# Performance work log

Measured on AMD Instinct MI355X. Metric: run time of the kernel, lower is better.

Reference implementation:

```python
import jax, jax.numpy as jnp
import numpy as np

N_USERS = 100000
N_MOVIES = 20000
N_EDGES = 600000
FEAT = 64
HID = 128
OUT = 64
N_TUPLES = 100000


def _sage(x_src, x_dst, src_idx, dst_idx, n_dst, Wl, bl, Wr):
    # PyG SAGEConv (mean aggr): lin_l(mean of gathered src feats) + lin_r(x_dst)
    msg = x_src[src_idx]                                        # [E, d_src]
    summ = jax.ops.segment_sum(msg, dst_idx, num_segments=n_dst)
    cnt = jax.ops.segment_sum(jnp.ones((src_idx.shape[0],), x_src.dtype),
                              dst_idx, num_segments=n_dst)
    mean = summ / jnp.maximum(cnt, 1.0)[:, None]
    return mean @ Wl.T + bl + x_dst @ Wr.T


def setup_inputs() -> dict:
    key = jax.random.key(0)
    ks = jax.random.split(key, 20)
    s = 0.05
    return {
        "movie_x": jax.random.normal(ks[0], (N_MOVIES, FEAT), jnp.float32),
        "user_idx": jax.random.randint(ks[1], (N_EDGES,), 0, N_USERS),
        "movie_idx": jax.random.randint(ks[2], (N_EDGES,), 0, N_MOVIES),
        "tuples_coo": jax.random.randint(ks[3], (2, N_TUPLES), 0, N_MOVIES),
        "user_emb": jax.random.normal(ks[4], (1, HID), jnp.float32) * s,
        "W1l": jax.random.normal(ks[5], (HID, FEAT), jnp.float32) * s,
        "b1": jnp.zeros((HID,), jnp.float32),
        "W1r": jax.random.normal(ks[6], (HID, HID), jnp.float32) * s,
        "W2l": jax.random.normal(ks[7], (HID, HID), jnp.float32) * s,
        "b2": jnp.zeros((HID,), jnp.float32),
        "W2r": jax.random.normal(ks[8], (HID, FEAT), jnp.float32) * s,
        "W3l": jax.random.normal(ks[9], (HID, HID), jnp.float32) * s,
        "b3": jnp.zeros((HID,), jnp.float32),
        "W3r": jax.random.normal(ks[10], (HID, HID), jnp.float32) * s,
        "Wlin1": jax.random.normal(ks[11], (OUT, HID), jnp.float32) * s,
        "blin1": jnp.zeros((OUT,), jnp.float32),
        "Wlin2": jax.random.normal(ks[12], (OUT, HID), jnp.float32) * s,
        "blin2": jnp.zeros((OUT,), jnp.float32),
    }


def reference(movie_x, user_idx, movie_idx, tuples_coo, user_emb,
              W1l, b1, W1r, W2l, b2, W2r, W3l, b3, W3r,
              Wlin1, blin1, Wlin2, blin2):
    n_users = N_USERS
    user_x0 = jnp.broadcast_to(user_emb, (n_users, HID))  # emb.weight.repeat
    # conv1: (movie -> user) rev_rates edges: src=movie_idx, dst=user_idx
    user_x = jax.nn.relu(_sage(movie_x, user_x0, movie_idx, user_idx, n_users, W1l, b1, W1r))
    # conv2: (user -> movie) rates edges: src=user_idx, dst=movie_idx
    movie_z = jax.nn.relu(_sage(user_x, movie_x, user_idx, movie_idx, N_MOVIES, W2l, b2, W2r))
    # conv3: (movie -> user) again
    user_z = jax.nn.relu(_sage(movie_z, user_x, movie_idx, user_idx, n_users, W3l, b3, W3r))
    z_user = user_z @ Wlin1.T + blin1
    z_movie = movie_z @ Wlin2.T + blin2
    X = jnp.vstack((z_user, z_movie))
    # relation_schema = ['user', 'movie']: offset movie indices by n_users
    new_index = jnp.vstack((tuples_coo[0], tuples_coo[1] + n_users))
    return X, new_index
```

## Files before the change

kernel.cpp:

```cpp
#include <hip/hip_runtime.h>

typedef __attribute__((ext_vector_type(8))) short short8;
typedef __attribute__((ext_vector_type(4))) float f32x4;

static const int NU = 100000;
static const int NM = 20000;
static const int NE = 600000;
static const int FEAT = 64;
static const int HID = 128;
static const int OUTD = 64;
static const int NTOT = NU + NM;
static const int CVT_TOT = 81920 + NM * FEAT;
static const int CVT_BLKS = (CVT_TOT + 255) / 256;
static const int IDX_BLKS = (100000 + 255) / 256;

static const int UB_SHIFT = 9;
static const int MB_SHIFT = 7;
static const int NBU = (NU + 511) >> 9;
static const int NBM = (NM + 127) >> 7;
static const int NBUCK = NBU + NBM;
static const int EPB = 4096;
static const int NPBLK = (NE + EPB - 1) / EPB;
static const int CAP = 8192;
static const int Y1_BLKS = (NM + 127) / 128;
static const int GB2 = (NM + 15) / 16;
static const int T3_BLKS = (NU + 127) / 128;

__device__ inline float b2f(unsigned short h) {
    unsigned int u = ((unsigned int)h) << 16;
    float f; __builtin_memcpy(&f, &u, 4); return f;
}
__device__ inline unsigned short f2b(float f) {
    unsigned int u; __builtin_memcpy(&u, &f, 4);
    u += 0x7FFFu + ((u >> 16) & 1u);
    return (unsigned short)(u >> 16);
}
__device__ inline unsigned int pk2(float a, float b) {
    return (unsigned int)f2b(a) | ((unsigned int)f2b(b) << 16);
}
__device__ inline int wswz(int row, int bc, int rowbytes) {
    return row * rowbytes + (bc ^ ((row & 7) << 4));
}

__global__ __launch_bounds__(256) void k_part_misc(
        const int* __restrict__ ui, const int* __restrict__ mi,
        int* __restrict__ gcur, int* __restrict__ entries,
        const float* __restrict__ w1l, const float* __restrict__ w2l,
        const float* __restrict__ w2r, const float* __restrict__ w3l,
        const float* __restrict__ w3r, const float* __restrict__ wl1,
        const float* __restrict__ wl2, const float* __restrict__ mx,
        unsigned short* __restrict__ dst,
        const int* __restrict__ tpl, float* __restrict__ oidx,
        const float* __restrict__ ue, const float* __restrict__ w1r,
        const float* __restrict__ b1, float* __restrict__ c1) {
    __shared__ int h[NBUCK], base[NBUCK], cur[NBUCK];
    const int b = blockIdx.x;
    const int tid = threadIdx.x;
    if (b < NPBLK) {
        for (int i = tid; i < NBUCK; i += 256) h[i] = 0;
        __syncthreads();
        int eu[EPB / 256], em[EPB / 256];
#pragma unroll
        for (int it = 0; it < EPB / 256; ++it) {
            int e = b * EPB + it * 256 + tid;
            if (e < NE) {
                eu[it] = ui[e]; em[it] = mi[e];
                atomicAdd(&h[eu[it] >> UB_SHIFT], 1);
                atomicAdd(&h[NBU + (em[it] >> MB_SHIFT)], 1);
            } else eu[it] = -1;
        }
        __syncthreads();
        for (int i = tid; i < NBUCK; i += 256) {
            int c = h[i];
            base[i] = c ? (i * CAP + atomicAdd(&gcur[i], c)) : 0;
            cur[i] = 0;
        }
        __syncthreads();
#pragma unroll
        for (int it = 0; it < EPB / 256; ++it) {
            if (eu[it] < 0) continue;
            int u = eu[it], m = em[it];
            int bu = u >> UB_SHIFT;
            int o1 = base[bu] + atomicAdd(&cur[bu], 1);
            entries[o1] = (m << UB_SHIFT) | (u & 511);
            int bm = NBU + (m >> MB_SHIFT);
            int o2 = base[bm] + atomicAdd(&cur[bm], 1);
            entries[o2] = (u << MB_SHIFT) | (m & 127);
        }
    } else if (b < NPBLK + CVT_BLKS) {
        int g = (b - NPBLK) * 256 + tid;
        if (g >= CVT_TOT) return;
        const float* s; int o;
        if      (g < 8192)   { s = w1l; o = g; }
        else if (g < 24576)  { s = w2l; o = g - 8192; }
        else if (g < 32768)  { s = w2r; o = g - 24576; }
        else if (g < 49152)  { s = w3l; o = g - 32768; }
        else if (g < 65536)  { s = w3r; o = g - 49152; }
        else if (g < 73728)  { s = wl1; o = g - 65536; }
        else if (g < 81920)  { s = wl2; o = g - 73728; }
        else                 { s = mx;  o = g - 81920; }
        dst[g] = f2b(s[o]);
    } else if (b < NPBLK + CVT_BLKS + IDX_BLKS) {
        int i = (b - NPBLK - CVT_BLKS) * 256 + tid;
        if (i < 100000) {
            oidx[i] = (float)tpl[i];
            oidx[100000 + i] = (float)(tpl[100000 + i] + NU);
        }
    } else {
        int hh = tid;
        if (hh < HID) {
            float a = 0.f;
#pragma unroll 16
            for (int k = 0; k < HID; ++k) a += ue[k] * w1r[hh * HID + k];
            c1[hh] = a + b1[hh];
        }
    }
}

__global__ __launch_bounds__(256) void k_csr_y1(
        const int* __restrict__ gcur, const int* __restrict__ entries,
        int2* __restrict__ rp2, int* __restrict__ list,
        const unsigned short* __restrict__ mxb, const unsigned short* __restrict__ W1l,
        unsigned short* __restrict__ Y1) {
    __shared__ __align__(16) char lds[16384];
    const int b = blockIdx.x;
    const int tid = threadIdx.x;
    if (b < NBUCK) {
        int* lcnt = (int*)lds;
        int* lrp  = lcnt + 512;
        int* lcur = lrp + 512;
        int* ps   = lcur + 512;
        const int s = b * CAP;
        const int e = s + gcur[b];
        const bool isU = b < NBU;
        const int shift = isU ? UB_SHIFT : MB_SHIFT;
        const int mask = isU ? 511 : 127;
        const int n0 = isU ? (b << UB_SHIFT) : ((b - NBU) << MB_SHIFT);
        const int nNodes = isU ? min(512, NU - n0) : min(128, NM - n0);
        const int g0 = isU ? n0 : NU + n0;

        for (int i = tid; i < 512; i += 256) { lcnt[i] = 0; lcur[i] = 0; }
        __syncthreads();
        for (int i = s + tid; i < e; i += 256)
            atomicAdd(&lcnt[entries[i] & mask], 1);
        __syncthreads();
        int a0 = lcnt[2 * tid], a1 = lcnt[2 * tid + 1];
        int pr = a0 + a1;
        ps[tid] = pr;
        __syncthreads();
#pragma unroll
        for (int off = 1; off < 256; off <<= 1) {
            int x = (tid >= off) ? ps[tid - off] : 0;
            __syncthreads();
            ps[tid] += x;
            __syncthreads();
        }
        int excl = ps[tid] - pr;
        lrp[2 * tid] = excl;
        lrp[2 * tid + 1] = excl + a0;
        __syncthreads();
        for (int i = tid; i < nNodes; i += 256)
            rp2[g0 + i] = make_int2(s + lrp[i], s + lrp[i] + lcnt[i]);
        for (int i = s + tid; i < e; i += 256) {
            int p = entries[i];
            int dl = p & mask;
            int off = s + lrp[dl] + atomicAdd(&lcur[dl], 1);
            list[off] = p >> shift;
        }
    } else {
        const int gb = b - NBUCK;
        const int lane = tid & 63;
        const int wv = tid >> 6;
        const int rbase = gb * 128 + wv * 32;
        const int lr = lane & 15;
        const int kg = lane >> 4;
#pragma unroll
        for (int i = 0; i < 4; ++i) {
            int idx = tid + i * 256;
            int row = idx >> 3, bc = (idx & 7) << 4;
            *reinterpret_cast<uint4*>(lds + wswz(row, bc, 128)) =
                *reinterpret_cast<const uint4*>((const char*)W1l + idx * 16);
        }
        short8 xb[2][2];
#pragma unroll
        for (int t = 0; t < 2; ++t) {
            int row = min(rbase + t * 16 + lr, NM - 1);
#pragma unroll
            for (int kt = 0; kt < 2; ++kt)
                xb[t][kt] = *reinterpret_cast<const short8*>(
                    mxb + (size_t)row * FEAT + kt * 32 + kg * 8);
        }
        __syncthreads();
        f32x4 acc[2][8];
#pragma unroll
        for (int t = 0; t < 2; ++t)
#pragma unroll
            for (int c = 0; c < 8; ++c) acc[t][c] = (f32x4){0.f, 0.f, 0.f, 0.f};
#pragma unroll
        for (int cg = 0; cg < 8; ++cg) {
            short8 wf[2];
#pragma unroll
            for (int kt = 0; kt < 2; ++kt)
                wf[kt] = *reinterpret_cast<const short8*>(
                    lds + wswz(cg * 16 + lr, kt * 64 + kg * 16, 128));
#pragma unroll
            for (int kt = 0; kt < 2; ++kt)
#pragma unroll
                for (int t = 0; t < 2; ++t)
                    acc[t][cg] = __builtin_amdgcn_mfma_f32_16x16x32_bf16(
                        wf[kt], xb[t][kt], acc[t][cg], 0, 0, 0);
        }
#pragma unroll
        for (int t = 0; t < 2; ++t) {
            const int u = rbase + t * 16 + lr;
            if (u >= NM) continue;
#pragma unroll
            for (int cg = 0; cg < 8; ++cg) {
                const int h0 = cg * 16 + kg * 4;
                uint2 o = make_uint2(pk2(acc[t][cg][0], acc[t][cg][1]),
                                     pk2(acc[t][cg][2], acc[t][cg][3]));
                *reinterpret_cast<uint2*>(Y1 + (size_t)u * HID + h0) = o;
            }
        }
    }
}

__global__ __launch_bounds__(256) void k_gather_relu(const unsigned short* __restrict__ Y1,
                                                     const int2* __restrict__ rp2,
                                                     const int* __restrict__ list,
                                                     const float* __restrict__ c1,
                                                     unsigned short* __restrict__ user_x,
                                                     int n) {
    const int node = blockIdx.x * 16 + threadIdx.x / 16;
    if (node >= n) return;
    const int c8 = (threadIdx.x % 16) * 8;
    const int2 se = rp2[node];
    const int s = se.x, e = se.y;

    float a[8];
#pragma unroll
    for (int j = 0; j < 8; ++j) a[j] = 0.f;
    int i = s;
    for (; i + 3 < e; i += 4) {
        int r0 = list[i], r1 = list[i + 1], r2 = list[i + 2], r3 = list[i + 3];
        short8 v0 = *reinterpret_cast<const short8*>(Y1 + (size_t)r0 * HID + c8);
        short8 v1 = *reinterpret_cast<const short8*>(Y1 + (size_t)r1 * HID + c8);
        short8 v2 = *reinterpret_cast<const short8*>(Y1 + (size_t)r2 * HID + c8);
        short8 v3 = *reinterpret_cast<const short8*>(Y1 + (size_t)r3 * HID + c8);
#pragma unroll
        for (int j = 0; j < 8; ++j)
            a[j] += (b2f((unsigned short)v0[j]) + b2f((unsigned short)v1[j]))
                  + (b2f((unsigned short)v2[j]) + b2f((unsigned short)v3[j]));
    }
    for (; i < e; ++i) {
        int r0 = list[i];
        short8 v0 = *reinterpret_cast<const short8*>(Y1 + (size_t)r0 * HID + c8);
#pragma unroll
        for (int j = 0; j < 8; ++j) a[j] += b2f((unsigned short)v0[j]);
    }
    const float sc = 1.0f / (float)max(e - s, 1);
    float4 cv0 = *reinterpret_cast<const float4*>(c1 + c8);
    float4 cv1 = *reinterpret_cast<const float4*>(c1 + c8 + 4);
    float r[8];
    r[0] = fmaxf(a[0] * sc + cv0.x, 0.f); r[1] = fmaxf(a[1] * sc + cv0.y, 0.f);
    r[2] = fmaxf(a[2] * sc + cv0.z, 0.f); r[3] = fmaxf(a[3] * sc + cv0.w, 0.f);
    r[4] = fmaxf(a[4] * sc + cv1.x, 0.f); r[5] = fmaxf(a[5] * sc + cv1.y, 0.f);
    r[6] = fmaxf(a[6] * sc + cv1.z, 0.f); r[7] = fmaxf(a[7] * sc + cv1.w, 0.f);
    uint4 o;
    o.x = pk2(r[0], r[1]); o.y = pk2(r[2], r[3]);
    o.z = pk2(r[4], r[5]); o.w = pk2(r[6], r[7]);
    *reinterpret_cast<uint4*>(user_x + (size_t)node * HID + c8) = o;
}

__global__ __launch_bounds__(256) void k_g2t3(
        const unsigned short* __restrict__ user_x, const int2* __restrict__ rp2,
        const int* __restrict__ list, unsigned short* __restrict__ mean2,
        const unsigned short* __restrict__ W3r, const float* __restrict__ b3,
        unsigned short* __restrict__ T3) {
    __shared__ __align__(16) char lds[32768];
    const int b = blockIdx.x;
    const int tid = threadIdx.x;
    if (b < GB2) {
        const int node = b * 16 + tid / 16;
        if (node >= NM) return;
        const int c8 = (tid % 16) * 8;
        const int2 se = rp2[NU + node];
        const int s = se.x, e = se.y;
        float a[8];
#pragma unroll
        for (int j = 0; j < 8; ++j) a[j] = 0.f;
        int i = s;
        for (; i + 3 < e; i += 4) {
            int r0 = list[i], r1 = list[i + 1], r2 = list[i + 2], r3 = list[i + 3];
            short8 v0 = *reinterpret_cast<const short8*>(user_x + (size_t)r0 * HID + c8);
            short8 v1 = *reinterpret_cast<const short8*>(user_x + (size_t)r1 * HID + c8);
            short8 v2 = *reinterpret_cast<const short8*>(user_x + (size_t)r2 * HID + c8);
            short8 v3 = *reinterpret_cast<const short8*>(user_x + (size_t)r3 * HID + c8);
#pragma unroll
            for (int j = 0; j < 8; ++j)
                a[j] += (b2f((unsigned short)v0[j]) + b2f((unsigned short)v1[j]))
                      + (b2f((unsigned short)v2[j]) + b2f((unsigned short)v3[j]));
        }
        for (; i < e; ++i) {
            int r0 = list[i];
            short8 v0 = *reinterpret_cast<const short8*>(user_x + (size_t)r0 * HID + c8);
#pragma unroll
            for (int j = 0; j < 8; ++j) a[j] += b2f((unsigned short)v0[j]);
        }
        const float sc = 1.0f / (float)max(e - s, 1);
        short8 o;
#pragma unroll
        for (int j = 0; j < 8; ++j) o[j] = (short)f2b(a[j] * sc);
        *reinterpret_cast<short8*>(mean2 + (size_t)node * HID + c8) = o;
    } else {
        const int gb = b - GB2;
        const int lane = tid & 63;
        const int wv = tid >> 6;
        const int rbase = gb * 128 + wv * 32;
        const int lr = lane & 15;
        const int kg = lane >> 4;
#pragma unroll
        for (int i = 0; i < 8; ++i) {
            int idx = tid + i * 256;
            int row = idx >> 4, bc = (idx & 15) << 4;
            *reinterpret_cast<uint4*>(lds + wswz(row, bc, 256)) =
                *reinterpret_cast<const uint4*>((const char*)W3r + idx * 16);
        }
        short8 xb[2][4];
#pragma unroll
        for (int t = 0; t < 2; ++t) {
            int row = min(rbase + t * 16 + lr, NU - 1);
#pragma unroll
            for (int kt = 0; kt < 4; ++kt)
                xb[t][kt] = *reinterpret_cast<const short8*>(
                    user_x + (size_t)row * HID + kt * 32 + kg * 8);
        }
        __syncthreads();
        f32x4 acc[2][8];
#pragma unroll
        for (int t = 0; t < 2; ++t)
#pragma unroll
            for (int c = 0; c < 8; ++c) acc[t][c] = (f32x4){0.f, 0.f, 0.f, 0.f};
#pragma unroll
        for (int cg = 0; cg < 8; ++cg) {
            short8 wf[4];
#pragma unroll
            for (int kt = 0; kt < 4; ++kt)
                wf[kt] = *reinterpret_cast<const short8*>(
                    lds + wswz(cg * 16 + lr, kt * 64 + kg * 16, 256));
#pragma unroll
            for (int kt = 0; kt < 4; ++kt)
#pragma unroll
                for (int t = 0; t < 2; ++t)
                    acc[t][cg] = __builtin_amdgcn_mfma_f32_16x16x32_bf16(
                        wf[kt], xb[t][kt], acc[t][cg], 0, 0, 0);
        }
#pragma unroll
        for (int t = 0; t < 2; ++t) {
            const int u = rbase + t * 16 + lr;
            if (u >= NU) continue;
#pragma unroll
            for (int cg = 0; cg < 8; ++cg) {
                const int h0 = cg * 16 + kg * 4;
                float4 vv = *reinterpret_cast<const float4*>(b3 + h0);
                uint2 o = make_uint2(pk2(acc[t][cg][0] + vv.x, acc[t][cg][1] + vv.y),
                                     pk2(acc[t][cg][2] + vv.z, acc[t][cg][3] + vv.w));
                *reinterpret_cast<uint2*>(T3 + (size_t)u * HID + h0) = o;
            }
        }
    }
}

__global__ __launch_bounds__(256) void k_gather_z(const unsigned short* __restrict__ Y3,
                                                  const int2* __restrict__ rp2,
                                                  const int* __restrict__ list,
                                                  const unsigned short* __restrict__ T3,
                                                  unsigned short* __restrict__ Z, int n) {
    const int node = blockIdx.x * 16 + threadIdx.x / 16;
    if (node >= n) return;
    const int c8 = (threadIdx.x % 16) * 8;
    const int2 se = rp2[node];
    const int s = se.x, e = se.y;

    float a[8];
#pragma unroll
    for (int j = 0; j < 8; ++j) a[j] = 0.f;
    int i = s;
    for (; i + 3 < e; i += 4) {
        int r0 = list[i], r1 = list[i + 1], r2 = list[i + 2], r3 = list[i + 3];
        short8 v0 = *reinterpret_cast<const short8*>(Y3 + (size_t)r0 * HID + c8);
        short8 v1 = *reinterpret_cast<const short8*>(Y3 + (size_t)r1 * HID + c8);
        short8 v2 = *reinterpret_cast<const short8*>(Y3 + (size_t)r2 * HID + c8);
        short8 v3 = *reinterpret_cast<const short8*>(Y3 + (size_t)r3 * HID + c8);
#pragma unroll
        for (int j = 0; j < 8; ++j)
            a[j] += (b2f((unsigned short)v0[j]) + b2f((unsigned short)v1[j]))
                  + (b2f((unsigned short)v2[j]) + b2f((unsigned short)v3[j]));
    }
    for (; i < e; ++i) {
        int r0 = list[i];
        short8 v0 = *reinterpret_cast<const short8*>(Y3 + (size_t)r0 * HID + c8);
#pragma unroll
        for (int j = 0; j < 8; ++j) a[j] += b2f((unsigned short)v0[j]);
    }
    const float sc = 1.0f / (float)max(e - s, 1);
    short8 t3 = *reinterpret_cast<const short8*>(T3 + (size_t)node * HID + c8);
    short8 o;
#pragma unroll
    for (int j = 0; j < 8; ++j)
        o[j] = (short)f2b(fmaxf(a[j] * sc + b2f((unsigned short)t3[j]), 0.f));
    *reinterpret_cast<short8*>(Z + (size_t)node * HID + c8) = o;
}

template<int K, int NO, bool AVEC, bool RELU, bool F32OUT>
__global__ __launch_bounds__(256) void k_mf2(const unsigned short* __restrict__ X,
                                             const unsigned short* __restrict__ W,
                                             const float* __restrict__ vec,
                                             void* __restrict__ Yv, int M) {
    constexpr int KT = K / 32;
    constexpr int CG = NO / 16;
    constexpr int WB = NO * K * 2;
    constexpr int RB = K * 2;
    __shared__ __align__(16) char lds[WB];
    const int tid = threadIdx.x;
    const int lane = tid & 63;
    const int wv = tid >> 6;
    const int rbase = blockIdx.x * 128 + wv * 32;
    const int lr = lane & 15;
    const int kg = lane >> 4;

#pragma unroll
    for (int i = 0; i < WB / 16 / 256; ++i) {
        int idx = tid + i * 256;
        int row = idx / (RB / 16);
        int bc = (idx % (RB / 16)) * 16;
        *reinterpret_cast<uint4*>(lds + wswz(row, bc, RB)) =
            *reinterpret_cast<const uint4*>((const char*)W + idx * 16);
    }

    short8 xb[2][KT];
#pragma unroll
    for (int t = 0; t < 2; ++t) {
        int row = min(rbase + t * 16 + lr, M - 1);
#pragma unroll
        for (int kt = 0; kt < KT; ++kt)
            xb[t][kt] = *reinterpret_cast<const short8*>(
                X + (size_t)row * K + kt * 32 + kg * 8);
    }
    __syncthreads();

    f32x4 acc[2][CG];
#pragma unroll
    for (int t = 0; t < 2; ++t)
#pragma unroll
        for (int c = 0; c < CG; ++c) acc[t][c] = (f32x4){0.f, 0.f, 0.f, 0.f};

#pragma unroll
    for (int cg = 0; cg < CG; ++cg) {
        short8 wf[KT];
#pragma unroll
        for (int kt = 0; kt < KT; ++kt)
            wf[kt] = *reinterpret_cast<const short8*>(
                lds + wswz(cg * 16 + lr, kt * 64 + kg * 16, RB));
#pragma unroll
        for (int kt = 0; kt < KT; ++kt)
#pragma unroll
            for (int t = 0; t < 2; ++t)
                acc[t][cg] = __builtin_amdgcn_mfma_f32_16x16x32_bf16(
                    wf[kt], xb[t][kt], acc[t][cg], 0, 0, 0);
    }

#pragma unroll
    for (int t = 0; t < 2; ++t) {
        const int u = rbase + t * 16 + lr;
        if (u >= M) continue;
#pragma unroll
        for (int cg = 0; cg < CG; ++cg) {
            const int h0 = cg * 16 + kg * 4;
            float v[4];
#pragma unroll
            for (int r = 0; r < 4; ++r) v[r] = acc[t][cg][r];
            if (AVEC) {
                float4 vv = *reinterpret_cast<const float4*>(vec + h0);
                v[0] += vv.x; v[1] += vv.y; v[2] += vv.z; v[3] += vv.w;
            }
            if (RELU)
#pragma unroll
                for (int r = 0; r < 4; ++r) v[r] = fmaxf(v[r], 0.f);
            if (F32OUT) {
                float4 o = make_float4(v[0], v[1], v[2], v[3]);
                *reinterpret_cast<float4*>((float*)Yv + (size_t)u * NO + h0) = o;
            } else {
                uint2 o = make_uint2(pk2(v[0], v[1]), pk2(v[2], v[3]));
                *reinterpret_cast<uint2*>((unsigned short*)Yv + (size_t)u * NO + h0) = o;
            }
        }
    }
}

__global__ __launch_bounds__(256) void k_fused_m(
        const unsigned short* __restrict__ mean2, const unsigned short* __restrict__ mxb,
        const unsigned short* __restrict__ W2l, const unsigned short* __restrict__ W2r,
        const float* __restrict__ b2, unsigned short* __restrict__ movie_z,
        const unsigned short* __restrict__ Wl2, const float* __restrict__ bl2,
        const unsigned short* __restrict__ W3l, unsigned short* __restrict__ Y3,
        float* __restrict__ out, int M) {
    __shared__ __align__(16) char lds[65536];
    const int tid = threadIdx.x;
    const int lane = tid & 63;
    const int wv = tid >> 6;
    const int rbase = blockIdx.x * 128 + wv * 32;
    const int lr = lane & 15;
    const int kg = lane >> 4;

#pragma unroll
    for (int i = 0; i < 8; ++i) {
        int idx = tid + i * 256;
        int row = idx >> 4, bc = (idx & 15) << 4;
        *reinterpret_cast<uint4*>(lds + wswz(row, bc, 256)) =
            *reinterpret_cast<const uint4*>((const char*)W2l + idx * 16);
    }
#pragma unroll
    for (int i = 0; i < 4; ++i) {
        int idx = tid + i * 256;
        int row = idx >> 3, bc = (idx & 7) << 4;
        *reinterpret_cast<uint4*>(lds + 32768 + wswz(row, bc, 128)) =
            *reinterpret_cast<const uint4*>((const char*)W2r + idx * 16);
        int row2 = idx >> 4, bc2 = (idx & 15) << 4;
        *reinterpret_cast<uint4*>(lds + 49152 + wswz(row2, bc2, 256)) =
            *reinterpret_cast<const uint4*>((const char*)Wl2 + idx * 16);
    }

    short8 xa[2][4], xc[2][2];
#pragma unroll
    for (int t = 0; t < 2; ++t) {
        int row = min(rbase + t * 16 + lr, M - 1);
#pragma unroll
        for (int kt = 0; kt < 4; ++kt)
            xa[t][kt] = *reinterpret_cast<const short8*>(
                mean2 + (size_t)row * HID + kt * 32 + kg * 8);
#pragma unroll
        for (int kt = 0; kt < 2; ++kt)
            xc[t][kt] = *reinterpret_cast<const short8*>(
                mxb + (size_t)row * FEAT + kt * 32 + kg * 8);
    }
    __syncthreads();

    f32x4 acc[2][8];
#pragma unroll
    for (int t = 0; t < 2; ++t)
#pragma unroll
        for (int c = 0; c < 8; ++c) acc[t][c] = (f32x4){0.f, 0.f, 0.f, 0.f};

#pragma unroll
    for (int cg = 0; cg < 8; ++cg) {
        short8 wl[4], wr[2];
#pragma unroll
        for (int kt = 0; kt < 4; ++kt)
            wl[kt] = *reinterpret_cast<const short8*>(
                lds + wswz(cg * 16 + lr, kt * 64 + kg * 16, 256));
#pragma unroll
        for (int kt = 0; kt < 2; ++kt)
            wr[kt] = *reinterpret_cast<const short8*>(
                lds + 32768 + wswz(cg * 16 + lr, kt * 64 + kg * 16, 128));
#pragma unroll
        for (int kt = 0; kt < 4; ++kt)
#pragma unroll
            for (int t = 0; t < 2; ++t)
                acc[t][cg] = __builtin_amdgcn_mfma_f32_16x16x32_bf16(
                    wl[kt], xa[t][kt], acc[t][cg], 0, 0, 0);
#pragma unroll
        for (int kt = 0; kt < 2; ++kt)
#pragma unroll
            for (int t = 0; t < 2; ++t)
                acc[t][cg] = __builtin_amdgcn_mfma_f32_16x16x32_bf16(
                    wr[kt], xc[t][kt], acc[t][cg], 0, 0, 0);
    }
    __syncthreads();

#pragma unroll
    for (int t = 0; t < 2; ++t) {
        const int ul = wv * 32 + t * 16 + lr;
        const int u = rbase + t * 16 + lr;
#pragma unroll
        for (int cg = 0; cg < 8; ++cg) {
            const int h0 = cg * 16 + kg * 4;
            float4 vv = *reinterpret_cast<const float4*>(b2 + h0);
            float v0 = fmaxf(acc[t][cg][0] + vv.x, 0.f);
            float v1 = fmaxf(acc[t][cg][1] + vv.y, 0.f);
            float v2 = fmaxf(acc[t][cg][2] + vv.z, 0.f);
            float v3 = fmaxf(acc[t][cg][3] + vv.w, 0.f);
            uint2 pk = make_uint2(pk2(v0, v1), pk2(v2, v3));
            *reinterpret_cast<uint2*>(lds + wswz(ul, h0 * 2, 256)) = pk;
            if (u < M)
                *reinterpret_cast<uint2*>(movie_z + (size_t)u * HID + h0) = pk;
        }
    }
    __syncthreads();

    short8 zb[2][4];
#pragma unroll
    for (int t = 0; t < 2; ++t) {
        const int ul = wv * 32 + t * 16 + lr;
#pragma unroll
        for (int kt = 0; kt < 4; ++kt)
            zb[t][kt] = *reinterpret_cast<const short8*>(
                lds + wswz(ul, kt * 64 + kg * 16, 256));
    }
    f32x4 a2[2][4];
#pragma unroll
    for (int t = 0; t < 2; ++t)
#pragma unroll
        for (int c = 0; c < 4; ++c) a2[t][c] = (f32x4){0.f, 0.f, 0.f, 0.f};
#pragma unroll
    for (int cg = 0; cg < 4; ++cg) {
        short8 wf[4];
#pragma unroll
        for (int kt = 0; kt < 4; ++kt)
            wf[kt] = *reinterpret_cast<const short8*>(
                lds + 49152 + wswz(cg * 16 + lr, kt * 64 + kg * 16, 256));
#pragma unroll
        for (int kt = 0; kt < 4; ++kt)
#pragma unroll
            for (int t = 0; t < 2; ++t)
                a2[t][cg] = __builtin_amdgcn_mfma_f32_16x16x32_bf16(
                    wf[kt], zb[t][kt], a2[t][cg], 0, 0, 0);
    }
#pragma unroll
    for (int t = 0; t < 2; ++t) {
        const int u = rbase + t * 16 + lr;
        if (u >= M) continue;
#pragma unroll
        for (int cg = 0; cg < 4; ++cg) {
            const int o0 = cg * 16 + kg * 4;
            float4 bb = *reinterpret_cast<const float4*>(bl2 + o0);
            float4 o = make_float4(a2[t][cg][0] + bb.x, a2[t][cg][1] + bb.y,
                                   a2[t][cg][2] + bb.z, a2[t][cg][3] + bb.w);
            *reinterpret_cast<float4*>(out + (size_t)u * OUTD + o0) = o;
        }
    }
    __syncthreads();

#pragma unroll
    for (int i = 0; i < 8; ++i) {
        int idx = tid + i * 256;
        int row = idx >> 4, bc = (idx & 15) << 4;
        *reinterpret_cast<uint4*>(lds + 32768 + wswz(row, bc, 256)) =
            *reinterpret_cast<const uint4*>((const char*)W3l + idx * 16);
    }
    __syncthreads();

    f32x4 a3[2][8];
#pragma unroll
    for (int t = 0; t < 2; ++t)
#pragma unroll
        for (int c = 0; c < 8; ++c) a3[t][c] = (f32x4){0.f, 0.f, 0.f, 0.f};
#pragma unroll
    for (int cg = 0; cg < 8; ++cg) {
        short8 wf[4];
#pragma unroll
        for (int kt = 0; kt < 4; ++kt)
            wf[kt] = *reinterpret_cast<const short8*>(
                lds + 32768 + wswz(cg * 16 + lr, kt * 64 + kg * 16, 256));
#pragma unroll
        for (int kt = 0; kt < 4; ++kt)
#pragma unroll
            for (int t = 0; t < 2; ++t)
                a3[t][cg] = __builtin_amdgcn_mfma_f32_16x16x32_bf16(
                    wf[kt], zb[t][kt], a3[t][cg], 0, 0, 0);
    }
#pragma unroll
    for (int t = 0; t < 2; ++t) {
        const int u = rbase + t * 16 + lr;
        if (u >= M) continue;
#pragma unroll
        for (int cg = 0; cg < 8; ++cg) {
            const int h0 = cg * 16 + kg * 4;
            uint2 pk = make_uint2(pk2(a3[t][cg][0], a3[t][cg][1]),
                                  pk2(a3[t][cg][2], a3[t][cg][3]));
            *reinterpret_cast<uint2*>(Y3 + (size_t)u * HID + h0) = pk;
        }
    }
}

extern "C" void kernel_launch(void* const* d_in, const int* in_sizes, int n_in,
                              void* d_out, int out_size, void* d_ws, size_t ws_size,
                              hipStream_t stream) {
    const float* movie_x  = (const float*)d_in[0];
    const int*   user_idx = (const int*)d_in[1];
    const int*   movie_idx= (const int*)d_in[2];
    const int*   tuples   = (const int*)d_in[3];
    const float* user_emb = (const float*)d_in[4];
    const float* W1l = (const float*)d_in[5];
    const float* b1  = (const float*)d_in[6];
    const float* W1r = (const float*)d_in[7];
    const float* W2l = (const float*)d_in[8];
    const float* b2  = (const float*)d_in[9];
    const float* W2r = (const float*)d_in[10];
    const float* W3l = (const float*)d_in[11];
    const float* b3  = (const float*)d_in[12];
    const float* W3r = (const float*)d_in[13];
    const float* Wlin1 = (const float*)d_in[14];
    const float* blin1 = (const float*)d_in[15];
    const float* Wlin2 = (const float*)d_in[16];
    const float* blin2 = (const float*)d_in[17];

    float* out = (float*)d_out;

    char* p = (char*)d_ws;
    int* gcur = (int*)p;  p += 360 * 4;
    int* entries = (int*)p; p += (size_t)NBUCK * CAP * 4;
    int2* rp2  = (int2*)p; p += (size_t)NTOT * 8;
    int* list  = (int*)p;  p += (size_t)NBUCK * CAP * 4;
    float* c1  = (float*)p; p += 128 * 4;
    unsigned short* wb = (unsigned short*)p; p += (size_t)CVT_TOT * 2;
    unsigned short* W1l_b  = wb;
    unsigned short* W2l_b  = wb + 8192;
    unsigned short* W2r_b  = wb + 24576;
    unsigned short* W3l_b  = wb + 32768;
    unsigned short* W3r_b  = wb + 49152;
    unsigned short* Wlin1_b= wb + 65536;
    unsigned short* Wlin2_b= wb + 73728;
    unsigned short* mxb    = wb + 81920;
    unsigned short* Y1     = (unsigned short*)p; p += (size_t)NM * HID * 2;
    unsigned short* user_x = (unsigned short*)p; p += (size_t)NU * HID * 2;
    unsigned short* mean2  = (unsigned short*)p; p += (size_t)NM * HID * 2;
    unsigned short* movie_z= (unsigned short*)p; p += (size_t)NM * HID * 2;
    unsigned short* Y3     = (unsigned short*)p; p += (size_t)NM * HID * 2;
    unsigned short* T3     = (unsigned short*)p; p += (size_t)NU * HID * 2;
    unsigned short* Z      = (unsigned short*)p; p += (size_t)NU * HID * 2;

    hipMemsetAsync(gcur, 0, NBUCK * sizeof(int), stream);
    k_part_misc<<<NPBLK + CVT_BLKS + IDX_BLKS + 1, 256, 0, stream>>>(
        user_idx, movie_idx, gcur, entries,
        W1l, W2l, W2r, W3l, W3r, Wlin1, Wlin2, movie_x, wb,
        tuples, out + (size_t)(NU + NM) * OUTD, user_emb, W1r, b1, c1);

    k_csr_y1<<<NBUCK + Y1_BLKS, 256, 0, stream>>>(gcur, entries, rp2, list,
                                                  mxb, W1l_b, Y1);

    k_gather_relu<<<(NU + 15) / 16, 256, 0, stream>>>(Y1, rp2, list, c1, user_x, NU);

    k_g2t3<<<GB2 + T3_BLKS, 256, 0, stream>>>(user_x, rp2, list, mean2, W3r_b, b3, T3);

    k_fused_m<<<(NM + 127) / 128, 256, 0, stream>>>(
        mean2, mxb, W2l_b, W2r_b, b2, movie_z, Wlin2_b, blin2, W3l_b, Y3,
        out + (size_t)NU * OUTD, NM);

    k_gather_z<<<(NU + 15) / 16, 256, 0, stream>>>(Y3, rp2, list, T3, Z, NU);

    k_mf2<HID, OUTD, true, false, true><<<(NU + 127) / 128, 256, 0, stream>>>(
        Z, Wlin1_b, blin1, out, NU);
}
```

Measured before the change: 165.9 us.

## Move T3 matmul into fused movie kernel and unroll mean2 gather by 8

The user-side T3 = user_x·W3rᵀ GEMM used to share a launch with the movie mean2 gather. It now shares a launch with the fused movie GEMM kernel instead, and the gather gets its own kernel. That kernel unrolls by 8 to keep more independent loads in flight. The aim is to balance the work mix across launches and hide gather latency. The cost is that the fused kernel now has a larger grid sharing 64KB of LDS per block, which may lower occupancy for the T3 blocks.

```diff
diff --git a/kernel.cpp b/kernel.cpp
--- a/kernel.cpp
+++ b/kernel.cpp
@@ -23,7 +23,7 @@
 static const int NPBLK = (NE + EPB - 1) / EPB;
 static const int CAP = 8192;
 static const int Y1_BLKS = (NM + 127) / 128;
-static const int GB2 = (NM + 15) / 16;
+static const int FM_BLKS = (NM + 127) / 128;
 static const int T3_BLKS = (NU + 127) / 128;
 
 __device__ inline float b2f(unsigned short h) {
@@ -272,103 +272,53 @@
     *reinterpret_cast<uint4*>(user_x + (size_t)node * HID + c8) = o;
 }
 
-__global__ __launch_bounds__(256) void k_g2t3(
-        const unsigned short* __restrict__ user_x, const int2* __restrict__ rp2,
-        const int* __restrict__ list, unsigned short* __restrict__ mean2,
-        const unsigned short* __restrict__ W3r, const float* __restrict__ b3,
-        unsigned short* __restrict__ T3) {
-    __shared__ __align__(16) char lds[32768];
-    const int b = blockIdx.x;
-    const int tid = threadIdx.x;
-    if (b < GB2) {
-        const int node = b * 16 + tid / 16;
-        if (node >= NM) return;
-        const int c8 = (tid % 16) * 8;
-        const int2 se = rp2[NU + node];
-        const int s = se.x, e = se.y;
-        float a[8];
-#pragma unroll
-        for (int j = 0; j < 8; ++j) a[j] = 0.f;
-        int i = s;
-        for (; i + 3 < e; i += 4) {
-            int r0 = list[i], r1 = list[i + 1], r2 = list[i + 2], r3 = list[i + 3];
-            short8 v0 = *reinterpret_cast<const short8*>(user_x + (size_t)r0 * HID + c8);
-            short8 v1 = *reinterpret_cast<const short8*>(user_x + (size_t)r1 * HID + c8);
-            short8 v2 = *reinterpret_cast<const short8*>(user_x + (size_t)r2 * HID + c8);
-            short8 v3 = *reinterpret_cast<const short8*>(user_x + (size_t)r3 * HID + c8);
+__global__ __launch_bounds__(256) void k_gather8(const unsigned short* __restrict__ src,
+                                                 const int2* __restrict__ rp2,
+                                                 const int* __restrict__ list,
+                                                 unsigned short* __restrict__ dst,
+                                                 int base, int n) {
+    const int node = blockIdx.x * 16 + threadIdx.x / 16;
+    if (node >= n) return;
+    const int c8 = (threadIdx.x % 16) * 8;
+    const int2 se = rp2[base + node];
+    const int s = se.x, e = se.y;
+
+    float a[8];
+#pragma unroll
+    for (int j = 0; j < 8; ++j) a[j] = 0.f;
+    int i = s;
+    for (; i + 7 < e; i += 8) {
+        short8 v[8];
+#pragma unroll
+        for (int q = 0; q < 8; ++q)
+            v[q] = *reinterpret_cast<const short8*>(src + (size_t)list[i + q] * HID + c8);
+#pragma unroll
+        for (int q = 0; q < 8; ++q)
 #pragma unroll
             for (int j = 0; j < 8; ++j)
-                a[j] += (b2f((unsigned short)v0[j]) + b2f((unsigned short)v1[j]))
-                      + (b2f((unsigned short)v2[j]) + b2f((unsigned short)v3[j]));
-        }
-        for (; i < e; ++i) {
-            int r0 = list[i];
-            short8 v0 = *reinterpret_cast<const short8*>(user_x + (size_t)r0 * HID + c8);
-#pragma unroll
-            for (int j = 0; j < 8; ++j) a[j] += b2f((unsigned short)v0[j]);
-        }
-        const float sc = 1.0f / (float)max(e - s, 1);
-        short8 o;
-#pragma unroll
-        for (int j = 0; j < 8; ++j) o[j] = (short)f2b(a[j] * sc);
-        *reinterpret_cast<short8*>(mean2 + (size_t)node * HID + c8) = o;
-    } else {
-        const int gb = b - GB2;
-        const int lane = tid & 63;
-        const int wv = tid >> 6;
-        const int rbase = gb * 128 + wv * 32;
-        const int lr = lane & 15;
-        const int kg = lane >> 4;
-#pragma unroll
-        for (int i = 0; i < 8; ++i) {
-            int idx = tid + i * 256;
-            int row = idx >> 4, bc = (idx & 15) << 4;
-            *reinterpret_cast<uint4*>(lds + wswz(row, bc, 256)) =
-                *reinterpret_cast<const uint4*>((const char*)W3r + idx * 16);
-        }
-        short8 xb[2][4];
-#pragma unroll
-        for (int t = 0; t < 2; ++t) {
-            int row = min(rbase + t * 16 + lr, NU - 1);
-#pragma unroll
-            for (int kt = 0; kt < 4; ++kt)
-                xb[t][kt] = *reinterpret_cast<const short8*>(
-                    user_x + (size_t)row * HID + kt * 32 + kg * 8);
-        }
-        __syncthreads();
-        f32x4 acc[2][8];
-#pragma unroll
-        for (int t = 0; t < 2; ++t)
-#pragma unroll
-            for (int c = 0; c < 8; ++c) acc[t][c] = (f32x4){0.f, 0.f, 0.f, 0.f};
-#pragma unroll
-        for (int cg = 0; cg < 8; ++cg) {
-            short8 wf[4];
-#pragma unroll
-            for (int kt = 0; kt < 4; ++kt)
-                wf[kt] = *reinterpret_cast<const short8*>(
-                    lds + wswz(cg * 16 + lr, kt * 64 + kg * 16, 256));
-#pragma unroll
-            for (int kt = 0; kt < 4; ++kt)
-#pragma unroll
-                for (int t = 0; t < 2; ++t)
-                    acc[t][cg] = __builtin_amdgcn_mfma_f32_16x16x32_bf16(
-                        wf[kt], xb[t][kt], acc[t][cg], 0, 0, 0);
-        }
-#pragma unroll
-        for (int t = 0; t < 2; ++t) {
-            const int u = rbase + t * 16 + lr;
-            if (u >= NU) continue;
-#pragma unroll
-            for (int cg = 0; cg < 8; ++cg) {
-                const int h0 = cg * 16 + kg * 4;
-                float4 vv = *reinterpret_cast<const float4*>(b3 + h0);
-                uint2 o = make_uint2(pk2(acc[t][cg][0] + vv.x, acc[t][cg][1] + vv.y),
-                                     pk2(acc[t][cg][2] + vv.z, acc[t][cg][3] + vv.w));
-                *reinterpret_cast<uint2*>(T3 + (size_t)u * HID + h0) = o;
-            }
-        }
-    }
+                a[j] += b2f((unsigned short)v[q][j]);
+    }
+    for (; i + 3 < e; i += 4) {
+        short8 v[4];
+#pragma unroll
+        for (int q = 0; q < 4; ++q)
+            v[q] = *reinterpret_cast<const short8*>(src + (size_t)list[i + q] * HID + c8);
+#pragma unroll
+        for (int q = 0; q < 4; ++q)
+#pragma unroll
+            for (int j = 0; j < 8; ++j)
+                a[j] += b2f((unsigned short)v[q][j]);
+    }
+    for (; i < e; ++i) {
+        short8 v0 = *reinterpret_cast<const short8*>(src + (size_t)list[i] * HID + c8);
+#pragma unroll
+        for (int j = 0; j < 8; ++j) a[j] += b2f((unsigned short)v0[j]);
+    }
+    const float sc = 1.0f / (float)max(e - s, 1);
+    short8 o;
+#pragma unroll
+    for (int j = 0; j < 8; ++j) o[j] = (short)f2b(a[j] * sc);
+    *reinterpret_cast<short8*>(dst + (size_t)node * HID + c8) = o;
 }
 
 __global__ __launch_bounds__(256) void k_gather_z(const unsigned short* __restrict__ Y3,
@@ -498,21 +448,78 @@
     }
 }
 
-__global__ __launch_bounds__(256) void k_fused_m(
+__global__ __launch_bounds__(256) void k_fm_t3(
         const unsigned short* __restrict__ mean2, const unsigned short* __restrict__ mxb,
         const unsigned short* __restrict__ W2l, const unsigned short* __restrict__ W2r,
         const float* __restrict__ b2, unsigned short* __restrict__ movie_z,
         const unsigned short* __restrict__ Wl2, const float* __restrict__ bl2,
         const unsigned short* __restrict__ W3l, unsigned short* __restrict__ Y3,
-        float* __restrict__ out, int M) {
+        float* __restrict__ out, int M,
+        const unsigned short* __restrict__ user_x, const unsigned short* __restrict__ W3r,
+        const float* __restrict__ b3, unsigned short* __restrict__ T3) {
     __shared__ __align__(16) char lds[65536];
     const int tid = threadIdx.x;
     const int lane = tid & 63;
     const int wv = tid >> 6;
-    const int rbase = blockIdx.x * 128 + wv * 32;
     const int lr = lane & 15;
     const int kg = lane >> 4;
 
+    if (blockIdx.x >= FM_BLKS) {
+        const int gb = blockIdx.x - FM_BLKS;
+        const int rbase = gb * 128 + wv * 32;
+#pragma unroll
+        for (int i = 0; i < 8; ++i) {
+            int idx = tid + i * 256;
+            int row = idx >> 4, bc = (idx & 15) << 4;
+            *reinterpret_cast<uint4*>(lds + wswz(row, bc, 256)) =
+                *reinterpret_cast<const uint4*>((const char*)W3r + idx * 16);
+        }
+        short8 xb[2][4];
+#pragma unroll
+        for (int t = 0; t < 2; ++t) {
+            int row = min(rbase + t * 16 + lr, NU - 1);
+#pragma unroll
+            for (int kt = 0; kt < 4; ++kt)
+                xb[t][kt] = *reinterpret_cast<const short8*>(
+                    user_x + (size_t)row * HID + kt * 32 + kg * 8);
+        }
+        __syncthreads();
+        f32x4 acc[2][8];
+#pragma unroll
+        for (int t = 0; t < 2; ++t)
+#pragma unroll
+            for (int c = 0; c < 8; ++c) acc[t][c] = (f32x4){0.f, 0.f, 0.f, 0.f};
+#pragma unroll
+        for (int cg = 0; cg < 8; ++cg) {
+            short8 wf[4];
+#pragma unroll
+            for (int kt = 0; kt < 4; ++kt)
+                wf[kt] = *reinterpret_cast<const short8*>(
+                    lds + wswz(cg * 16 + lr, kt * 64 + kg * 16, 256));
+#pragma unroll
+            for (int kt = 0; kt < 4; ++kt)
+#pragma unroll
+                for (int t = 0; t < 2; ++t)
+                    acc[t][cg] = __builtin_amdgcn_mfma_f32_16x16x32_bf16(
+                        wf[kt], xb[t][kt], acc[t][cg], 0, 0, 0);
+        }
+#pragma unroll
+        for (int t = 0; t < 2; ++t) {
+            const int u = rbase + t * 16 + lr;
+            if (u >= NU) continue;
+#pragma unroll
+            for (int cg = 0; cg < 8; ++cg) {
+                const int h0 = cg * 16 + kg * 4;
+                float4 vv = *reinterpret_cast<const float4*>(b3 + h0);
+                uint2 o = make_uint2(pk2(acc[t][cg][0] + vv.x, acc[t][cg][1] + vv.y),
+                                     pk2(acc[t][cg][2] + vv.z, acc[t][cg][3] + vv.w));
+                *reinterpret_cast<uint2*>(T3 + (size_t)u * HID + h0) = o;
+            }
+        }
+        return;
+    }
+
+    const int rbase = blockIdx.x * 128 + wv * 32;
 #pragma unroll
     for (int i = 0; i < 8; ++i) {
         int idx = tid + i * 256;
@@ -741,11 +748,11 @@
 
     k_gather_relu<<<(NU + 15) / 16, 256, 0, stream>>>(Y1, rp2, list, c1, user_x, NU);
 
-    k_g2t3<<<GB2 + T3_BLKS, 256, 0, stream>>>(user_x, rp2, list, mean2, W3r_b, b3, T3);
-
-    k_fused_m<<<(NM + 127) / 128, 256, 0, stream>>>(
+    k_gather8<<<(NM + 15) / 16, 256, 0, stream>>>(user_x, rp2, list, mean2, NU, NM);
+
+    k_fm_t3<<<FM_BLKS + T3_BLKS, 256, 0, stream>>>(
         mean2, mxb, W2l_b, W2r_b, b2, movie_z, Wlin2_b, blin2, W3l_b, Y3,
-        out + (size_t)NU * OUTD, NM);
+        out + (size_t)NU * OUTD, NM, user_x, W3r_b, b3, T3);
 
     k_gather_z<<<(NU + 15) / 16, 256, 0, stream>>>(Y3, rp2, list, T3, Z, NU);
 
```

After: 161.3 us. 2.8% less time.
